# Kernel tuning notes

Measured on AMD Instinct MI355X. Metric: run time of the kernel, lower is better.

## Reference

```python
import jax, jax.numpy as jnp
import numpy as np

B, S, D = 2, 2048, 1024
H = 16
HD = D // H  # head_dim = 64


def setup_inputs() -> dict:
    key = jax.random.key(0)
    ks = jax.random.split(key, 9)
    sc_in = 1.0 / np.sqrt(D)
    return {
        "x": jax.random.normal(ks[0], (B, S, D), dtype=jnp.float32),
        "Wq": jax.random.normal(ks[1], (D, D), dtype=jnp.float32) * sc_in,
        "bq": jnp.zeros((D,), dtype=jnp.float32),
        "Wk": jax.random.normal(ks[2], (D, D), dtype=jnp.float32) * sc_in,
        "bk": jnp.zeros((D,), dtype=jnp.float32),
        "Wv": jax.random.normal(ks[3], (D, D), dtype=jnp.float32) * sc_in,
        "bv": jnp.zeros((D,), dtype=jnp.float32),
        "Wo": jax.random.normal(ks[4], (D, D), dtype=jnp.float32) * sc_in,
        "bo": jnp.zeros((D,), dtype=jnp.float32),
    }


def reference(x, Wq, bq, Wk, bk, Wv, bv, Wo, bo):
    # QKV projections: [B,S,D] -> [B,H,S,HD]
    def split_heads(t):
        return t.reshape(B, S, H, HD).transpose(0, 2, 1, 3)

    Q = split_heads(x @ Wq + bq)
    K = split_heads(x @ Wk + bk)
    V = split_heads(x @ Wv + bv)

    scale = 1.0 / np.sqrt(HD).astype(np.float32)
    scores = jnp.einsum("bhqd,bhkd->bhqk", Q, K) * scale  # [B,H,S,S]
    weights = jax.nn.softmax(scores, axis=-1)
    # dropout(p=0.1) is identity in eval mode
    attended = jnp.einsum("bhqk,bhkd->bhqd", weights, V)  # [B,H,S,HD]
    attended = attended.transpose(0, 2, 1, 3).reshape(B, S, D)
    return attended @ Wo + bo
```

## Files before the change

### kernel.cpp

```cpp
#include <hip/hip_runtime.h>
#include <hip/hip_bf16.h>


#define S_ 2048
#define D_ 1024
#define HD_ 64
#define LDSW 72
#define QSZ 4194304

typedef __attribute__((ext_vector_type(8))) short bf16x8;
typedef __attribute__((ext_vector_type(4))) float f32x4;

static __device__ __forceinline__ short f2bs(float f) {
    __hip_bfloat16 h = __float2bfloat16(f);
    return *reinterpret_cast<short*>(&h);
}
static __device__ __forceinline__ float bs2f(short s) {
    __hip_bfloat16 h = *reinterpret_cast<__hip_bfloat16*>(&s);
    return __bfloat162float(h);
}
static __device__ __forceinline__ bf16x8 cvt8(const float* p) {
    f32x4 u0 = *(const f32x4*)p;
    f32x4 u1 = *(const f32x4*)(p + 4);
    bf16x8 r;
    r[0] = f2bs(u0[0]); r[1] = f2bs(u0[1]); r[2] = f2bs(u0[2]); r[3] = f2bs(u0[3]);
    r[4] = f2bs(u1[0]); r[5] = f2bs(u1[1]); r[6] = f2bs(u1[2]); r[7] = f2bs(u1[3]);
    return r;
}
static __device__ __forceinline__ void gld16(const void* g, void* l) {
    __builtin_amdgcn_global_load_lds(
        (const __attribute__((address_space(1))) unsigned int*)g,
        (__attribute__((address_space(3))) unsigned int*)l, 16, 0, 0);
}
static __device__ __forceinline__ int detect_f32(const unsigned int* __restrict__ xw) {
    const unsigned int w = xw[threadIdx.x & 63];
    const int e = (int)((w >> 7) & 0xFFu);
    unsigned long long m = __ballot(e >= 117 && e <= 130);
    return (__popcll(m) >= 32) ? 0 : 1;
}

__global__ __launch_bounds__(256) void prep(
    const void* __restrict__ x,
    const void* __restrict__ w0, const void* __restrict__ w1,
    const void* __restrict__ w2, const void* __restrict__ w3,
    short* __restrict__ Wt, short* __restrict__ Xb)
{
    __shared__ __align__(16) short Ts[64 * LDSW];
    const int f32in = detect_f32((const unsigned int*)x);
    const int idx = blockIdx.x;

    if (idx >= 1024) {
        const int c = idx - 1024;
        const size_t base = (size_t)c * 8192 + (size_t)threadIdx.x * 8;
        if (f32in) {
            const float* xf = (const float*)x;
            #pragma unroll
            for (int i = 0; i < 4; ++i)
                *(bf16x8*)&Xb[base + (size_t)i * 2048] = cvt8(xf + base + (size_t)i * 2048);
        } else {
            const short* xs = (const short*)x;
            #pragma unroll
            for (int i = 0; i < 4; ++i)
                *(bf16x8*)&Xb[base + (size_t)i * 2048] = *(const bf16x8*)(xs + base + (size_t)i * 2048);
        }
        return;
    }

    const int z = idx >> 8, bb = idx & 255;
    const void* W = z == 0 ? w0 : z == 1 ? w1 : z == 2 ? w2 : w3;
    short* O = Wt + (size_t)z * D_ * D_;
    const int k0 = (bb & 15) * 64, n0 = (bb >> 4) * 64;
    const int t = threadIdx.x;
    const int row = t >> 2, seg = t & 3;

    if (f32in) {
        const float* wg = (const float*)W + (size_t)(k0 + row) * D_ + n0;
        *(bf16x8*)&Ts[row * LDSW + seg * 8]      = cvt8(wg + seg * 8);
        *(bf16x8*)&Ts[row * LDSW + seg * 8 + 32] = cvt8(wg + seg * 8 + 32);
    } else {
        const short* wg = (const short*)W + (size_t)(k0 + row) * D_ + n0;
        *(bf16x8*)&Ts[row * LDSW + seg * 8]      = *(const bf16x8*)(wg + seg * 8);
        *(bf16x8*)&Ts[row * LDSW + seg * 8 + 32] = *(const bf16x8*)(wg + seg * 8 + 32);
    }
    __syncthreads();

    short* og = O + (size_t)(n0 + row) * D_ + k0;
    #pragma unroll
    for (int g = 0; g < 2; ++g) {
        const int ks = seg * 8 + g * 32;
        alignas(16) short tmp[8];
        #pragma unroll
        for (int i = 0; i < 8; ++i) tmp[i] = Ts[(ks + i) * LDSW + row];
        *(bf16x8*)(og + ks) = *(const bf16x8*)tmp;
    }
}

__global__ __launch_bounds__(512) void gemm_qkv(
    const short* __restrict__ Xb, const short* __restrict__ Wt3,
    const void* __restrict__ bq, const void* __restrict__ bk,
    const void* __restrict__ bv, short* __restrict__ out,
    const unsigned int* __restrict__ xw)
{
    __shared__ __align__(16) short As[2][256 * 64];
    __shared__ __align__(16) short Bs[2][192 * 64];
    const int ext_f32 = detect_f32(xw);
    const int t = threadIdx.x;
    const int wave = t >> 6, lane = t & 63;
    const int quad = lane >> 4, l16 = lane & 15;
    const int wm = wave & 1, wn = wave >> 1;
    const int m0 = blockIdx.x * 256, n0 = blockIdx.y * 192;
    const int lr = lane >> 3;
    const int kx = ((lane & 7) ^ (lr & 7)) * 8;

    f32x4 acc[8][3];
    #pragma unroll
    for (int i = 0; i < 8; ++i)
        #pragma unroll
        for (int j = 0; j < 3; ++j) acc[i][j] = (f32x4){0.f, 0.f, 0.f, 0.f};

    const short* Ab = Xb  + (size_t)(m0 + wave * 32 + lr) * D_ + kx;
    const short* Bb = Wt3 + (size_t)(n0 + wave * 24 + lr) * D_ + kx;

    #pragma unroll
    for (int i = 0; i < 4; ++i)
        gld16(Ab + (size_t)i * 8 * D_, &As[0][(wave * 4 + i) * 512]);
    #pragma unroll
    for (int i = 0; i < 3; ++i)
        gld16(Bb + (size_t)i * 8 * D_, &Bs[0][(wave * 3 + i) * 512]);
    __syncthreads();

    for (int kb = 0; kb < 16; ++kb) {
        const int cur = kb & 1;
        if (kb < 15) {
            const int kn = (kb + 1) * 64;
            #pragma unroll
            for (int i = 0; i < 4; ++i)
                gld16(Ab + (size_t)i * 8 * D_ + kn, &As[cur ^ 1][(wave * 4 + i) * 512]);
            #pragma unroll
            for (int i = 0; i < 3; ++i)
                gld16(Bb + (size_t)i * 8 * D_ + kn, &Bs[cur ^ 1][(wave * 3 + i) * 512]);
        }

        #pragma unroll
        for (int ks = 0; ks < 2; ++ks) {
            const int sw = ((ks * 4 + quad) ^ (l16 & 7)) * 8;
            bf16x8 af[8], bfr[3];
            #pragma unroll
            for (int i = 0; i < 8; ++i)
                af[i]  = *(const bf16x8*)&As[cur][(wm * 128 + i * 16 + l16) * 64 + sw];
            #pragma unroll
            for (int i = 0; i < 3; ++i)
                bfr[i] = *(const bf16x8*)&Bs[cur][(wn * 48 + i * 16 + l16) * 64 + sw];
            #pragma unroll
            for (int mi = 0; mi < 8; ++mi)
                #pragma unroll
                for (int ni = 0; ni < 3; ++ni)
                    acc[mi][ni] = __builtin_amdgcn_mfma_f32_16x16x32_bf16(
                        af[mi], bfr[ni], acc[mi][ni], 0, 0, 0);
        }

        __syncthreads();
    }

    #pragma unroll
    for (int ni = 0; ni < 3; ++ni) {
        const int n = n0 + wn * 48 + ni * 16 + l16;
        const int id = n >> 10, nl = n & 1023, h = nl >> 6, d = nl & 63;
        const void* bias = id == 0 ? bq : id == 1 ? bk : bv;
        const float oscale = id == 0 ? 0.18033688011112042f : 1.0f;
        const float bvl = ext_f32 ? ((const float*)bias)[nl]
                                  : bs2f(((const short*)bias)[nl]);
        #pragma unroll
        for (int mi = 0; mi < 8; ++mi)
            #pragma unroll
            for (int r = 0; r < 4; ++r) {
                const int m = m0 + wm * 128 + mi * 16 + quad * 4 + r;
                const int b = m >> 11, s = m & 2047;
                const int bh = b * 16 + h;
                const float v = (acc[mi][ni][r] + bvl) * oscale;
                const size_t idx = (id < 2)
                    ? (size_t)id * QSZ + ((size_t)bh * S_ + s) * HD_ + d
                    : (size_t)2 * QSZ + ((size_t)bh * HD_ + d) * S_ + s;
                out[idx] = f2bs(v);
            }
    }
}

__global__ __launch_bounds__(256) void gemm_out(
    const short* __restrict__ A, const short* __restrict__ Bt,
    const void* __restrict__ bias, void* __restrict__ C,
    const unsigned int* __restrict__ xw)
{
    __shared__ __align__(16) short As[2][64 * 64];
    __shared__ __align__(16) short Bs[2][128 * 64];
    const int ext_f32 = detect_f32(xw);
    const int t = threadIdx.x;
    const int wave = t >> 6, lane = t & 63;
    const int quad = lane >> 4, l16 = lane & 15;
    const int wm = wave & 1, wn = wave >> 1;
    const int m0 = blockIdx.x * 64, n0 = blockIdx.y * 128;
    const int lr = lane >> 3;
    const int kx = ((lane & 7) ^ (lr & 7)) * 8;

    f32x4 acc[2][4];
    #pragma unroll
    for (int i = 0; i < 2; ++i)
        #pragma unroll
        for (int j = 0; j < 4; ++j) acc[i][j] = (f32x4){0.f, 0.f, 0.f, 0.f};

    const short* Ab = A  + (size_t)(m0 + wave * 16 + lr) * D_ + kx;
    const short* Bb = Bt + (size_t)(n0 + wave * 32 + lr) * D_ + kx;

    #pragma unroll
    for (int i = 0; i < 2; ++i)
        gld16(Ab + (size_t)i * 8 * D_, &As[0][(wave * 2 + i) * 512]);
    #pragma unroll
    for (int i = 0; i < 4; ++i)
        gld16(Bb + (size_t)i * 8 * D_, &Bs[0][(wave * 4 + i) * 512]);
    __syncthreads();

    for (int kb = 0; kb < 16; ++kb) {
        const int cur = kb & 1;
        if (kb < 15) {
            const int kn = (kb + 1) * 64;
            #pragma unroll
            for (int i = 0; i < 2; ++i)
                gld16(Ab + (size_t)i * 8 * D_ + kn, &As[cur ^ 1][(wave * 2 + i) * 512]);
            #pragma unroll
            for (int i = 0; i < 4; ++i)
                gld16(Bb + (size_t)i * 8 * D_ + kn, &Bs[cur ^ 1][(wave * 4 + i) * 512]);
        }

        #pragma unroll
        for (int ks = 0; ks < 2; ++ks) {
            const int sw = ((ks * 4 + quad) ^ (l16 & 7)) * 8;
            bf16x8 af[2], bfr[4];
            #pragma unroll
            for (int i = 0; i < 2; ++i)
                af[i] = *(const bf16x8*)&As[cur][(wm * 32 + i * 16 + l16) * 64 + sw];
            #pragma unroll
            for (int i = 0; i < 4; ++i)
                bfr[i] = *(const bf16x8*)&Bs[cur][(wn * 64 + i * 16 + l16) * 64 + sw];
            #pragma unroll
            for (int mi = 0; mi < 2; ++mi)
                #pragma unroll
                for (int ni = 0; ni < 4; ++ni)
                    acc[mi][ni] = __builtin_amdgcn_mfma_f32_16x16x32_bf16(
                        af[mi], bfr[ni], acc[mi][ni], 0, 0, 0);
        }

        __syncthreads();
    }

    #pragma unroll
    for (int ni = 0; ni < 4; ++ni) {
        const int n = n0 + wn * 64 + ni * 16 + l16;
        const float bvl = ext_f32 ? ((const float*)bias)[n]
                                  : bs2f(((const short*)bias)[n]);
        #pragma unroll
        for (int mi = 0; mi < 2; ++mi)
            #pragma unroll
            for (int r = 0; r < 4; ++r) {
                const int m = m0 + wm * 32 + mi * 16 + quad * 4 + r;
                const float v = acc[mi][ni][r] + bvl;
                const size_t idx = (size_t)m * D_ + n;
                if (ext_f32) ((float*)C)[idx] = v;
                else         ((short*)C)[idx] = f2bs(v);
            }
    }
}

__global__ __launch_bounds__(512) void attn(
    const short* __restrict__ Q, const short* __restrict__ K,
    const short* __restrict__ Vt, short* __restrict__ Aout)
{
    __shared__ __align__(16) short Ks[2][64 * 64];
    __shared__ __align__(16) short Vs[2][64 * 64];
    __shared__ __align__(16) short Ps[8][16 * LDSW];

    const int t = threadIdx.x;
    const int wave = t >> 6, lane = t & 63;
    const int quad = lane >> 4, l16 = lane & 15;
    const int bh = blockIdx.x;
    const int q0 = blockIdx.y * 128;
    const int lr = lane >> 3;
    const int kx = ((lane & 7) ^ (lr & 7)) * 8;
    short* pw = &Ps[wave][0];

    bf16x8 bq0, bq1;
    {
        const short* qr = Q + ((size_t)bh * S_ + q0 + wave * 16 + l16) * HD_ + quad * 8;
        bq0 = *(const bf16x8*)qr;
        bq1 = *(const bf16x8*)(qr + 32);
    }

    bf16x8 ones;
    #pragma unroll
    for (int i = 0; i < 8; ++i) ones[i] = (short)0x3F80;

    f32x4 o[4], lacc;
    lacc = (f32x4){0.f, 0.f, 0.f, 0.f};
    #pragma unroll
    for (int nt = 0; nt < 4; ++nt) o[nt] = (f32x4){0.f, 0.f, 0.f, 0.f};

    const short* Kb = K  + ((size_t)bh * S_  + wave * 8 + lr) * HD_ + kx;
    const short* Vb = Vt + ((size_t)bh * HD_ + wave * 8 + lr) * S_ + kx;

    gld16(Kb, &Ks[0][wave * 512]);
    gld16(Vb, &Vs[0][wave * 512]);
    __syncthreads();

    for (int j = 0; j < 32; ++j) {
        const int cur = j & 1;
        if (j < 31) {
            gld16(Kb + (size_t)((j + 1) * 64) * HD_, &Ks[cur ^ 1][wave * 512]);
            gld16(Vb + (j + 1) * 64,                 &Vs[cur ^ 1][wave * 512]);
        }

        f32x4 st[4];
        #pragma unroll
        for (int nt = 0; nt < 4; ++nt) {
            bf16x8 kf0 = *(const bf16x8*)&Ks[cur][(nt * 16 + l16) * 64 + ((quad ^ (l16 & 7)) * 8)];
            bf16x8 kf1 = *(const bf16x8*)&Ks[cur][(nt * 16 + l16) * 64 + (((4 + quad) ^ (l16 & 7)) * 8)];
            f32x4 z = (f32x4){0.f, 0.f, 0.f, 0.f};
            z = __builtin_amdgcn_mfma_f32_16x16x32_bf16(kf0, bq0, z, 0, 0, 0);
            z = __builtin_amdgcn_mfma_f32_16x16x32_bf16(kf1, bq1, z, 0, 0, 0);
            st[nt] = z;
        }

        #pragma unroll
        for (int nt = 0; nt < 4; ++nt) {
            unsigned u0 = __float_as_uint(__builtin_amdgcn_exp2f(st[nt][0]));
            unsigned u1 = __float_as_uint(__builtin_amdgcn_exp2f(st[nt][1]));
            unsigned u2 = __float_as_uint(__builtin_amdgcn_exp2f(st[nt][2]));
            unsigned u3 = __float_as_uint(__builtin_amdgcn_exp2f(st[nt][3]));
            uint2 pk;
            pk.x = __builtin_amdgcn_perm(u1, u0, 0x07060302);
            pk.y = __builtin_amdgcn_perm(u3, u2, 0x07060302);
            *(uint2*)&pw[l16 * LDSW + nt * 16 + quad * 4] = pk;
        }
        __builtin_amdgcn_s_waitcnt(0xc07f);

        #pragma unroll
        for (int ks = 0; ks < 2; ++ks) {
            bf16x8 vf[4];
            #pragma unroll
            for (int nt = 0; nt < 4; ++nt)
                vf[nt] = *(const bf16x8*)&Vs[cur][(nt * 16 + l16) * 64 + (((ks * 4 + quad) ^ (l16 & 7)) * 8)];
            bf16x8 ap = *(const bf16x8*)&pw[l16 * LDSW + ks * 32 + quad * 8];
            lacc = __builtin_amdgcn_mfma_f32_16x16x32_bf16(ap, ones, lacc, 0, 0, 0);
            #pragma unroll
            for (int nt = 0; nt < 4; ++nt)
                o[nt] = __builtin_amdgcn_mfma_f32_16x16x32_bf16(ap, vf[nt], o[nt], 0, 0, 0);
        }

        __syncthreads();
    }

    const int b = bh >> 4, h = bh & 15;
    #pragma unroll
    for (int r = 0; r < 4; ++r) {
        const float inv = 1.f / lacc[r];
        const int s = q0 + wave * 16 + quad * 4 + r;
        const size_t base = ((size_t)b * S_ + s) * D_ + h * HD_;
        #pragma unroll
        for (int nt = 0; nt < 4; ++nt)
            Aout[base + nt * 16 + l16] = f2bs(o[nt][r] * inv);
    }
}

extern "C" void kernel_launch(void* const* d_in, const int* in_sizes, int n_in,
                              void* d_out, int out_size, void* d_ws, size_t ws_size,
                              hipStream_t stream) {
    char* ws = (char*)d_ws;
    short* Wt  = (short*)(ws + ((size_t)1  << 20));
    short* Att = (short*)(ws + ((size_t)9  << 20));
    short* Xb  = Att;
    short* QKV = (short*)(ws + ((size_t)17 << 20));
    const unsigned int* xw = (const unsigned int*)d_in[0];

    prep<<<1536, 256, 0, stream>>>(d_in[0], d_in[1], d_in[3], d_in[5], d_in[7], Wt, Xb);
    gemm_qkv<<<dim3(16, 16), 512, 0, stream>>>(Xb, Wt, d_in[2], d_in[4], d_in[6], QKV, xw);
    attn<<<dim3(32, 16), 512, 0, stream>>>(QKV, QKV + QSZ, QKV + 2 * QSZ, Att);
    gemm_out<<<dim3(64, 8), 256, 0, stream>>>(Att, Wt + (3 << 20), d_in[8], d_out, xw);
}
```

Measured before the change: 203.8 us.

## Fuse all four stages into one persistent cooperative kernel with grid syncs

Replaces the four separate launches (weight/input prep, QKV GEMM, attention, output GEMM) with a single cooperative kernel of 256 blocks that runs each stage in turn, separated by grid-wide barriers. The aim is to remove per-launch overhead and inter-kernel gaps. In exchange, the grid is fixed at 256 blocks with one 512-thread block per CU and 112 KB of shared LDS. This lowers parallelism in stages that previously used more blocks (attention and the output GEMM each had 512), and the output GEMM now runs 512 threads on tiles sized for 256.

```diff
diff --git a/kernel.cpp b/kernel.cpp
--- a/kernel.cpp
+++ b/kernel.cpp
@@ -1,5 +1,8 @@
 #include <hip/hip_runtime.h>
+#include <hip/hip_cooperative_groups.h>
 #include <hip/hip_bf16.h>
+
+namespace cg = cooperative_groups;
 
 
 #define S_ 2048
@@ -39,333 +42,317 @@
     return (__popcll(m) >= 32) ? 0 : 1;
 }
 
-__global__ __launch_bounds__(256) void prep(
+__global__ __launch_bounds__(512, 1) void mha_fused(
     const void* __restrict__ x,
-    const void* __restrict__ w0, const void* __restrict__ w1,
-    const void* __restrict__ w2, const void* __restrict__ w3,
-    short* __restrict__ Wt, short* __restrict__ Xb)
+    const void* __restrict__ Wq, const void* __restrict__ Wk,
+    const void* __restrict__ Wv, const void* __restrict__ Wo,
+    const void* __restrict__ bq, const void* __restrict__ bk,
+    const void* __restrict__ bv, const void* __restrict__ bo,
+    void* __restrict__ Cout,
+    short* __restrict__ Wt, short* __restrict__ XbAtt, short* __restrict__ QKV)
 {
-    __shared__ __align__(16) short Ts[64 * LDSW];
+    __shared__ __align__(16) short SB[57344];
+    cg::grid_group grid = cg::this_grid();
+
+    const int t = threadIdx.x;
+    const int blk = blockIdx.x;
+    const int wave = t >> 6, lane = t & 63;
+    const int quad = lane >> 4, l16 = lane & 15;
+    const int lr = lane >> 3;
+    const int kx = ((lane & 7) ^ (lr & 7)) * 8;
     const int f32in = detect_f32((const unsigned int*)x);
-    const int idx = blockIdx.x;
-
-    if (idx >= 1024) {
-        const int c = idx - 1024;
-        const size_t base = (size_t)c * 8192 + (size_t)threadIdx.x * 8;
+
+    {
+        const int sub = t >> 8, tt = t & 255;
+        const int row = tt >> 2, seg = tt & 3;
+        short* Ts = &SB[sub * 4608];
+        #pragma unroll
+        for (int u = 0; u < 2; ++u) {
+            const int unit = blk * 4 + sub * 2 + u;
+            const int z = unit >> 8, bb = unit & 255;
+            const void* W = z == 0 ? Wq : z == 1 ? Wk : z == 2 ? Wv : Wo;
+            short* O = Wt + (size_t)z * D_ * D_;
+            const int k0 = (bb & 15) * 64, n0 = (bb >> 4) * 64;
+            if (u) __syncthreads();
+            if (f32in) {
+                const float* wg = (const float*)W + (size_t)(k0 + row) * D_ + n0;
+                *(bf16x8*)&Ts[row * LDSW + seg * 8]      = cvt8(wg + seg * 8);
+                *(bf16x8*)&Ts[row * LDSW + seg * 8 + 32] = cvt8(wg + seg * 8 + 32);
+            } else {
+                const short* wg = (const short*)W + (size_t)(k0 + row) * D_ + n0;
+                *(bf16x8*)&Ts[row * LDSW + seg * 8]      = *(const bf16x8*)(wg + seg * 8);
+                *(bf16x8*)&Ts[row * LDSW + seg * 8 + 32] = *(const bf16x8*)(wg + seg * 8 + 32);
+            }
+            __syncthreads();
+            short* og = O + (size_t)(n0 + row) * D_ + k0;
+            #pragma unroll
+            for (int g = 0; g < 2; ++g) {
+                const int ks = seg * 8 + g * 32;
+                alignas(16) short tmp[8];
+                #pragma unroll
+                for (int i = 0; i < 8; ++i) tmp[i] = Ts[(ks + i) * LDSW + row];
+                *(bf16x8*)(og + ks) = *(const bf16x8*)tmp;
+            }
+        }
+        const size_t base = (size_t)blk * 16384 + (size_t)t * 8;
         if (f32in) {
             const float* xf = (const float*)x;
             #pragma unroll
             for (int i = 0; i < 4; ++i)
-                *(bf16x8*)&Xb[base + (size_t)i * 2048] = cvt8(xf + base + (size_t)i * 2048);
+                *(bf16x8*)&XbAtt[base + (size_t)i * 4096] = cvt8(xf + base + (size_t)i * 4096);
         } else {
             const short* xs = (const short*)x;
             #pragma unroll
             for (int i = 0; i < 4; ++i)
-                *(bf16x8*)&Xb[base + (size_t)i * 2048] = *(const bf16x8*)(xs + base + (size_t)i * 2048);
-        }
-        return;
+                *(bf16x8*)&XbAtt[base + (size_t)i * 4096] = *(const bf16x8*)(xs + base + (size_t)i * 4096);
+        }
     }
-
-    const int z = idx >> 8, bb = idx & 255;
-    const void* W = z == 0 ? w0 : z == 1 ? w1 : z == 2 ? w2 : w3;
-    short* O = Wt + (size_t)z * D_ * D_;
-    const int k0 = (bb & 15) * 64, n0 = (bb >> 4) * 64;
-    const int t = threadIdx.x;
-    const int row = t >> 2, seg = t & 3;
-
-    if (f32in) {
-        const float* wg = (const float*)W + (size_t)(k0 + row) * D_ + n0;
-        *(bf16x8*)&Ts[row * LDSW + seg * 8]      = cvt8(wg + seg * 8);
-        *(bf16x8*)&Ts[row * LDSW + seg * 8 + 32] = cvt8(wg + seg * 8 + 32);
-    } else {
-        const short* wg = (const short*)W + (size_t)(k0 + row) * D_ + n0;
-        *(bf16x8*)&Ts[row * LDSW + seg * 8]      = *(const bf16x8*)(wg + seg * 8);
-        *(bf16x8*)&Ts[row * LDSW + seg * 8 + 32] = *(const bf16x8*)(wg + seg * 8 + 32);
+    grid.sync();
+
+    {
+        short* As = SB;
+        short* Bs = SB + 32768;
+        const int wm = wave & 1, wn = wave >> 1;
+        const int m0 = (blk & 15) * 256, n0 = (blk >> 4) * 192;
+
+        f32x4 acc[8][3];
+        #pragma unroll
+        for (int i = 0; i < 8; ++i)
+            #pragma unroll
+            for (int j = 0; j < 3; ++j) acc[i][j] = (f32x4){0.f, 0.f, 0.f, 0.f};
+
+        const short* Ab = XbAtt + (size_t)(m0 + wave * 32 + lr) * D_ + kx;
+        const short* Bb = Wt    + (size_t)(n0 + wave * 24 + lr) * D_ + kx;
+
+        #pragma unroll
+        for (int i = 0; i < 4; ++i)
+            gld16(Ab + (size_t)i * 8 * D_, &As[(wave * 4 + i) * 512]);
+        #pragma unroll
+        for (int i = 0; i < 3; ++i)
+            gld16(Bb + (size_t)i * 8 * D_, &Bs[(wave * 3 + i) * 512]);
+        __syncthreads();
+
+        for (int kb = 0; kb < 16; ++kb) {
+            const int cur = kb & 1;
+            if (kb < 15) {
+                const int kn = (kb + 1) * 64;
+                #pragma unroll
+                for (int i = 0; i < 4; ++i)
+                    gld16(Ab + (size_t)i * 8 * D_ + kn, &As[(cur ^ 1) * 16384 + (wave * 4 + i) * 512]);
+                #pragma unroll
+                for (int i = 0; i < 3; ++i)
+                    gld16(Bb + (size_t)i * 8 * D_ + kn, &Bs[(cur ^ 1) * 12288 + (wave * 3 + i) * 512]);
+            }
+            #pragma unroll
+            for (int ks = 0; ks < 2; ++ks) {
+                const int sw = ((ks * 4 + quad) ^ (l16 & 7)) * 8;
+                bf16x8 af[8], bfr[3];
+                #pragma unroll
+                for (int i = 0; i < 8; ++i)
+                    af[i]  = *(const bf16x8*)&As[cur * 16384 + (wm * 128 + i * 16 + l16) * 64 + sw];
+                #pragma unroll
+                for (int i = 0; i < 3; ++i)
+                    bfr[i] = *(const bf16x8*)&Bs[cur * 12288 + (wn * 48 + i * 16 + l16) * 64 + sw];
+                #pragma unroll
+                for (int mi = 0; mi < 8; ++mi)
+                    #pragma unroll
+                    for (int ni = 0; ni < 3; ++ni)
+                        acc[mi][ni] = __builtin_amdgcn_mfma_f32_16x16x32_bf16(
+                            af[mi], bfr[ni], acc[mi][ni], 0, 0, 0);
+            }
+            __syncthreads();
+        }
+
+        #pragma unroll
+        for (int ni = 0; ni < 3; ++ni) {
+            const int n = n0 + wn * 48 + ni * 16 + l16;
+            const int id = n >> 10, nl = n & 1023, h = nl >> 6, d = nl & 63;
+            const void* bias = id == 0 ? bq : id == 1 ? bk : bv;
+            const float oscale = id == 0 ? 0.18033688011112042f : 1.0f;
+            const float bvl = f32in ? ((const float*)bias)[nl]
+                                    : bs2f(((const short*)bias)[nl]);
+            #pragma unroll
+            for (int mi = 0; mi < 8; ++mi)
+                #pragma unroll
+                for (int r = 0; r < 4; ++r) {
+                    const int m = m0 + wm * 128 + mi * 16 + quad * 4 + r;
+                    const int b = m >> 11, s = m & 2047;
+                    const int bh = b * 16 + h;
+                    const float v = (acc[mi][ni][r] + bvl) * oscale;
+                    const size_t idx = (id < 2)
+                        ? (size_t)id * QSZ + ((size_t)bh * S_ + s) * HD_ + d
+                        : (size_t)2 * QSZ + ((size_t)bh * HD_ + d) * S_ + s;
+                    QKV[idx] = f2bs(v);
+                }
+        }
     }
-    __syncthreads();
-
-    short* og = O + (size_t)(n0 + row) * D_ + k0;
-    #pragma unroll
-    for (int g = 0; g < 2; ++g) {
-        const int ks = seg * 8 + g * 32;
-        alignas(16) short tmp[8];
-        #pragma unroll
-        for (int i = 0; i < 8; ++i) tmp[i] = Ts[(ks + i) * LDSW + row];
-        *(bf16x8*)(og + ks) = *(const bf16x8*)tmp;
+    grid.sync();
+
+    {
+        short* Ks = SB;
+        short* Vs = SB + 8192;
+        short* Ps = SB + 16384;
+        const short* Q  = QKV;
+        const short* K  = QKV + QSZ;
+        const short* Vt = QKV + 2 * QSZ;
+        short* pw = &Ps[wave * (16 * LDSW)];
+
+        #pragma unroll 1
+        for (int u = 0; u < 2; ++u) {
+            const int unit = blk * 2 + u;
+            const int bh = unit & 31, q0 = (unit >> 5) * 128;
+
+            bf16x8 bq0, bq1;
+            {
+                const short* qr = Q + ((size_t)bh * S_ + q0 + wave * 16 + l16) * HD_ + quad * 8;
+                bq0 = *(const bf16x8*)qr;
+                bq1 = *(const bf16x8*)(qr + 32);
+            }
+            bf16x8 ones;
+            #pragma unroll
+            for (int i = 0; i < 8; ++i) ones[i] = (short)0x3F80;
+
+            f32x4 o[4], lacc;
+            lacc = (f32x4){0.f, 0.f, 0.f, 0.f};
+            #pragma unroll
+            for (int nt = 0; nt < 4; ++nt) o[nt] = (f32x4){0.f, 0.f, 0.f, 0.f};
+
+            const short* Kb = K  + ((size_t)bh * S_  + wave * 8 + lr) * HD_ + kx;
+            const short* Vb = Vt + ((size_t)bh * HD_ + wave * 8 + lr) * S_ + kx;
+
+            gld16(Kb, &Ks[wave * 512]);
+            gld16(Vb, &Vs[wave * 512]);
+            __syncthreads();
+
+            for (int j = 0; j < 32; ++j) {
+                const int cur = j & 1;
+                if (j < 31) {
+                    gld16(Kb + (size_t)((j + 1) * 64) * HD_, &Ks[(cur ^ 1) * 4096 + wave * 512]);
+                    gld16(Vb + (j + 1) * 64,                 &Vs[(cur ^ 1) * 4096 + wave * 512]);
+                }
+
+                f32x4 st[4];
+                #pragma unroll
+                for (int nt = 0; nt < 4; ++nt) {
+                    bf16x8 kf0 = *(const bf16x8*)&Ks[cur * 4096 + (nt * 16 + l16) * 64 + ((quad ^ (l16 & 7)) * 8)];
+                    bf16x8 kf1 = *(const bf16x8*)&Ks[cur * 4096 + (nt * 16 + l16) * 64 + (((4 + quad) ^ (l16 & 7)) * 8)];
+                    f32x4 z = (f32x4){0.f, 0.f, 0.f, 0.f};
+                    z = __builtin_amdgcn_mfma_f32_16x16x32_bf16(kf0, bq0, z, 0, 0, 0);
+                    z = __builtin_amdgcn_mfma_f32_16x16x32_bf16(kf1, bq1, z, 0, 0, 0);
+                    st[nt] = z;
+                }
+
+                #pragma unroll
+                for (int nt = 0; nt < 4; ++nt) {
+                    unsigned u0 = __float_as_uint(__builtin_amdgcn_exp2f(st[nt][0]));
+                    unsigned u1 = __float_as_uint(__builtin_amdgcn_exp2f(st[nt][1]));
+                    unsigned u2 = __float_as_uint(__builtin_amdgcn_exp2f(st[nt][2]));
+                    unsigned u3 = __float_as_uint(__builtin_amdgcn_exp2f(st[nt][3]));
+                    uint2 pk;
+                    pk.x = __builtin_amdgcn_perm(u1, u0, 0x07060302);
+                    pk.y = __builtin_amdgcn_perm(u3, u2, 0x07060302);
+                    *(uint2*)&pw[l16 * LDSW + nt * 16 + quad * 4] = pk;
+                }
+                __builtin_amdgcn_s_waitcnt(0xc07f);
+
+                #pragma unroll
+                for (int ks = 0; ks < 2; ++ks) {
+                    bf16x8 vf[4];
+                    #pragma unroll
+                    for (int nt = 0; nt < 4; ++nt)
+                        vf[nt] = *(const bf16x8*)&Vs[cur * 4096 + (nt * 16 + l16) * 64 + (((ks * 4 + quad) ^ (l16 & 7)) * 8)];
+                    bf16x8 ap = *(const bf16x8*)&pw[l16 * LDSW + ks * 32 + quad * 8];
+                    lacc = __builtin_amdgcn_mfma_f32_16x16x32_bf16(ap, ones, lacc, 0, 0, 0);
+                    #pragma unroll
+                    for (int nt = 0; nt < 4; ++nt)
+                        o[nt] = __builtin_amdgcn_mfma_f32_16x16x32_bf16(ap, vf[nt], o[nt], 0, 0, 0);
+                }
+                __syncthreads();
+            }
+
+            const int b = bh >> 4, h = bh & 15;
+            #pragma unroll
+            for (int r = 0; r < 4; ++r) {
+                const float inv = 1.f / lacc[r];
+                const int s = q0 + wave * 16 + quad * 4 + r;
+                const size_t base = ((size_t)b * S_ + s) * D_ + h * HD_;
+                #pragma unroll
+                for (int nt = 0; nt < 4; ++nt)
+                    XbAtt[base + nt * 16 + l16] = f2bs(o[nt][r] * inv);
+            }
+        }
     }
-}
-
-__global__ __launch_bounds__(512) void gemm_qkv(
-    const short* __restrict__ Xb, const short* __restrict__ Wt3,
-    const void* __restrict__ bq, const void* __restrict__ bk,
-    const void* __restrict__ bv, short* __restrict__ out,
-    const unsigned int* __restrict__ xw)
-{
-    __shared__ __align__(16) short As[2][256 * 64];
-    __shared__ __align__(16) short Bs[2][192 * 64];
-    const int ext_f32 = detect_f32(xw);
-    const int t = threadIdx.x;
-    const int wave = t >> 6, lane = t & 63;
-    const int quad = lane >> 4, l16 = lane & 15;
-    const int wm = wave & 1, wn = wave >> 1;
-    const int m0 = blockIdx.x * 256, n0 = blockIdx.y * 192;
-    const int lr = lane >> 3;
-    const int kx = ((lane & 7) ^ (lr & 7)) * 8;
-
-    f32x4 acc[8][3];
-    #pragma unroll
-    for (int i = 0; i < 8; ++i)
-        #pragma unroll
-        for (int j = 0; j < 3; ++j) acc[i][j] = (f32x4){0.f, 0.f, 0.f, 0.f};
-
-    const short* Ab = Xb  + (size_t)(m0 + wave * 32 + lr) * D_ + kx;
-    const short* Bb = Wt3 + (size_t)(n0 + wave * 24 + lr) * D_ + kx;
-
-    #pragma unroll
-    for (int i = 0; i < 4; ++i)
-        gld16(Ab + (size_t)i * 8 * D_, &As[0][(wave * 4 + i) * 512]);
-    #pragma unroll
-    for (int i = 0; i < 3; ++i)
-        gld16(Bb + (size_t)i * 8 * D_, &Bs[0][(wave * 3 + i) * 512]);
-    __syncthreads();
-
-    for (int kb = 0; kb < 16; ++kb) {
-        const int cur = kb & 1;
-        if (kb < 15) {
-            const int kn = (kb + 1) * 64;
-            #pragma unroll
-            for (int i = 0; i < 4; ++i)
-                gld16(Ab + (size_t)i * 8 * D_ + kn, &As[cur ^ 1][(wave * 4 + i) * 512]);
-            #pragma unroll
-            for (int i = 0; i < 3; ++i)
-                gld16(Bb + (size_t)i * 8 * D_ + kn, &Bs[cur ^ 1][(wave * 3 + i) * 512]);
-        }
-
-        #pragma unroll
-        for (int ks = 0; ks < 2; ++ks) {
-            const int sw = ((ks * 4 + quad) ^ (l16 & 7)) * 8;
-            bf16x8 af[8], bfr[3];
-            #pragma unroll
-            for (int i = 0; i < 8; ++i)
-                af[i]  = *(const bf16x8*)&As[cur][(wm * 128 + i * 16 + l16) * 64 + sw];
-            #pragma unroll
-            for (int i = 0; i < 3; ++i)
-                bfr[i] = *(const bf16x8*)&Bs[cur][(wn * 48 + i * 16 + l16) * 64 + sw];
-            #pragma unroll
-            for (int mi = 0; mi < 8; ++mi)
-                #pragma unroll
-                for (int ni = 0; ni < 3; ++ni)
-                    acc[mi][ni] = __builtin_amdgcn_mfma_f32_16x16x32_bf16(
-                        af[mi], bfr[ni], acc[mi][ni], 0, 0, 0);
-        }
-
+    grid.sync();
+
+    {
+        short* As = SB;
+        short* Bs = SB + 16384;
+        const int wm = wave & 3, wn = wave >> 2;
+        const int m0 = (blk & 31) * 128, n0 = (blk >> 5) * 128;
+        const short* Bt = Wt + ((size_t)3 << 20);
+
+        f32x4 acc[2][4];
+        #pragma unroll
+        for (int i = 0; i < 2; ++i)
+            #pragma unroll
+            for (int j = 0; j < 4; ++j) acc[i][j] = (f32x4){0.f, 0.f, 0.f, 0.f};
+
+        const short* Ab = XbAtt + (size_t)(m0 + wave * 16 + lr) * D_ + kx;
+        const short* Bb = Bt    + (size_t)(n0 + wave * 16 + lr) * D_ + kx;
+
+        #pragma unroll
+        for (int i = 0; i < 2; ++i) {
+            gld16(Ab + (size_t)i * 8 * D_, &As[(wave * 2 + i) * 512]);
+            gld16(Bb + (size_t)i * 8 * D_, &Bs[(wave * 2 + i) * 512]);
+        }
         __syncthreads();
-    }
-
-    #pragma unroll
-    for (int ni = 0; ni < 3; ++ni) {
-        const int n = n0 + wn * 48 + ni * 16 + l16;
-        const int id = n >> 10, nl = n & 1023, h = nl >> 6, d = nl & 63;
-        const void* bias = id == 0 ? bq : id == 1 ? bk : bv;
-        const float oscale = id == 0 ? 0.18033688011112042f : 1.0f;
-        const float bvl = ext_f32 ? ((const float*)bias)[nl]
-                                  : bs2f(((const short*)bias)[nl]);
-        #pragma unroll
-        for (int mi = 0; mi < 8; ++mi)
-            #pragma unroll
-            for (int r = 0; r < 4; ++r) {
-                const int m = m0 + wm * 128 + mi * 16 + quad * 4 + r;
-                const int b = m >> 11, s = m & 2047;
-                const int bh = b * 16 + h;
-                const float v = (acc[mi][ni][r] + bvl) * oscale;
-                const size_t idx = (id < 2)
-                    ? (size_t)id * QSZ + ((size_t)bh * S_ + s) * HD_ + d
-                    : (size_t)2 * QSZ + ((size_t)bh * HD_ + d) * S_ + s;
-                out[idx] = f2bs(v);
-            }
-    }
-}
-
-__global__ __launch_bounds__(256) void gemm_out(
-    const short* __restrict__ A, const short* __restrict__ Bt,
-    const void* __restrict__ bias, void* __restrict__ C,
-    const unsigned int* __restrict__ xw)
-{
-    __shared__ __align__(16) short As[2][64 * 64];
-    __shared__ __align__(16) short Bs[2][128 * 64];
-    const int ext_f32 = detect_f32(xw);
-    const int t = threadIdx.x;
-    const int wave = t >> 6, lane = t & 63;
-    const int quad = lane >> 4, l16 = lane & 15;
-    const int wm = wave & 1, wn = wave >> 1;
-    const int m0 = blockIdx.x * 64, n0 = blockIdx.y * 128;
-    const int lr = lane >> 3;
-    const int kx = ((lane & 7) ^ (lr & 7)) * 8;
-
-    f32x4 acc[2][4];
-    #pragma unroll
-    for (int i = 0; i < 2; ++i)
-        #pragma unroll
-        for (int j = 0; j < 4; ++j) acc[i][j] = (f32x4){0.f, 0.f, 0.f, 0.f};
-
-    const short* Ab = A  + (size_t)(m0 + wave * 16 + lr) * D_ + kx;
-    const short* Bb = Bt + (size_t)(n0 + wave * 32 + lr) * D_ + kx;
-
-    #pragma unroll
-    for (int i = 0; i < 2; ++i)
-        gld16(Ab + (size_t)i * 8 * D_, &As[0][(wave * 2 + i) * 512]);
-    #pragma unroll
-    for (int i = 0; i < 4; ++i)
-        gld16(Bb + (size_t)i * 8 * D_, &Bs[0][(wave * 4 + i) * 512]);
-    __syncthreads();
-
-    for (int kb = 0; kb < 16; ++kb) {
-        const int cur = kb & 1;
-        if (kb < 15) {
-            const int kn = (kb + 1) * 64;
-            #pragma unroll
-            for (int i = 0; i < 2; ++i)
-                gld16(Ab + (size_t)i * 8 * D_ + kn, &As[cur ^ 1][(wave * 2 + i) * 512]);
-            #pragma unroll
-            for (int i = 0; i < 4; ++i)
-                gld16(Bb + (size_t)i * 8 * D_ + kn, &Bs[cur ^ 1][(wave * 4 + i) * 512]);
-        }
-
-        #pragma unroll
-        for (int ks = 0; ks < 2; ++ks) {
-            const int sw = ((ks * 4 + quad) ^ (l16 & 7)) * 8;
-            bf16x8 af[2], bfr[4];
-            #pragma unroll
-            for (int i = 0; i < 2; ++i)
-                af[i] = *(const bf16x8*)&As[cur][(wm * 32 + i * 16 + l16) * 64 + sw];
-            #pragma unroll
-            for (int i = 0; i < 4; ++i)
-                bfr[i] = *(const bf16x8*)&Bs[cur][(wn * 64 + i * 16 + l16) * 64 + sw];
+
+        for (int kb = 0; kb < 16; ++kb) {
+            const int cur = kb & 1;
+            if (kb < 15) {
+                const int kn = (kb + 1) * 64;
+                #pragma unroll
+                for (int i = 0; i < 2; ++i) {
+                    gld16(Ab + (size_t)i * 8 * D_ + kn, &As[(cur ^ 1) * 8192 + (wave * 2 + i) * 512]);
+                    gld16(Bb + (size_t)i * 8 * D_ + kn, &Bs[(cur ^ 1) * 8192 + (wave * 2 + i) * 512]);
+                }
+            }
+            #pragma unroll
+            for (int ks = 0; ks < 2; ++ks) {
+                const int sw = ((ks * 4 + quad) ^ (l16 & 7)) * 8;
+                bf16x8 af[2], bfr[4];
+                #pragma unroll
+                for (int i = 0; i < 2; ++i)
+                    af[i] = *(const bf16x8*)&As[cur * 8192 + (wm * 32 + i * 16 + l16) * 64 + sw];
+                #pragma unroll
+                for (int i = 0; i < 4; ++i)
+                    bfr[i] = *(const bf16x8*)&Bs[cur * 8192 + (wn * 64 + i * 16 + l16) * 64 + sw];
+                #pragma unroll
+                for (int mi = 0; mi < 2; ++mi)
+                    #pragma unroll
+                    for (int ni = 0; ni < 4; ++ni)
+                        acc[mi][ni] = __builtin_amdgcn_mfma_f32_16x16x32_bf16(
+                            af[mi], bfr[ni], acc[mi][ni], 0, 0, 0);
+            }
+            __syncthreads();
+        }
+
+        #pragma unroll
+        for (int ni = 0; ni < 4; ++ni) {
+            const int n = n0 + wn * 64 + ni * 16 + l16;
+            const float bvl = f32in ? ((const float*)bo)[n]
+                                    : bs2f(((const short*)bo)[n]);
             #pragma unroll
             for (int mi = 0; mi < 2; ++mi)
                 #pragma unroll
-                for (int ni = 0; ni < 4; ++ni)
-                    acc[mi][ni] = __builtin_amdgcn_mfma_f32_16x16x32_bf16(
-                        af[mi], bfr[ni], acc[mi][ni], 0, 0, 0);
-        }
-
-        __syncthreads();
-    }
-
-    #pragma unroll
-    for (int ni = 0; ni < 4; ++ni) {
-        const int n = n0 + wn * 64 + ni * 16 + l16;
-        const float bvl = ext_f32 ? ((const float*)bias)[n]
-                                  : bs2f(((const short*)bias)[n]);
-        #pragma unroll
-        for (int mi = 0; mi < 2; ++mi)
-            #pragma unroll
-            for (int r = 0; r < 4; ++r) {
-                const int m = m0 + wm * 32 + mi * 16 + quad * 4 + r;
-                const float v = acc[mi][ni][r] + bvl;
-                const size_t idx = (size_t)m * D_ + n;
-                if (ext_f32) ((float*)C)[idx] = v;
-                else         ((short*)C)[idx] = f2bs(v);
-            }
-    }
-}
-
-__global__ __launch_bounds__(512) void attn(
-    const short* __restrict__ Q, const short* __restrict__ K,
-    const short* __restrict__ Vt, short* __restrict__ Aout)
-{
-    __shared__ __align__(16) short Ks[2][64 * 64];
-    __shared__ __align__(16) short Vs[2][64 * 64];
-    __shared__ __align__(16) short Ps[8][16 * LDSW];
-
-    const int t = threadIdx.x;
-    const int wave = t >> 6, lane = t & 63;
-    const int quad = lane >> 4, l16 = lane & 15;
-    const int bh = blockIdx.x;
-    const int q0 = blockIdx.y * 128;
-    const int lr = lane >> 3;
-    const int kx = ((lane & 7) ^ (lr & 7)) * 8;
-    short* pw = &Ps[wave][0];
-
-    bf16x8 bq0, bq1;
-    {
-        const short* qr = Q + ((size_t)bh * S_ + q0 + wave * 16 + l16) * HD_ + quad * 8;
-        bq0 = *(const bf16x8*)qr;
-        bq1 = *(const bf16x8*)(qr + 32);
-    }
-
-    bf16x8 ones;
-    #pragma unroll
-    for (int i = 0; i < 8; ++i) ones[i] = (short)0x3F80;
-
-    f32x4 o[4], lacc;
-    lacc = (f32x4){0.f, 0.f, 0.f, 0.f};
-    #pragma unroll
-    for (int nt = 0; nt < 4; ++nt) o[nt] = (f32x4){0.f, 0.f, 0.f, 0.f};
-
-    const short* Kb = K  + ((size_t)bh * S_  + wave * 8 + lr) * HD_ + kx;
-    const short* Vb = Vt + ((size_t)bh * HD_ + wave * 8 + lr) * S_ + kx;
-
-    gld16(Kb, &Ks[0][wave * 512]);
-    gld16(Vb, &Vs[0][wave * 512]);
-    __syncthreads();
-
-    for (int j = 0; j < 32; ++j) {
-        const int cur = j & 1;
-        if (j < 31) {
-            gld16(Kb + (size_t)((j + 1) * 64) * HD_, &Ks[cur ^ 1][wave * 512]);
-            gld16(Vb + (j + 1) * 64,                 &Vs[cur ^ 1][wave * 512]);
-        }
-
-        f32x4 st[4];
-        #pragma unroll
-        for (int nt = 0; nt < 4; ++nt) {
-            bf16x8 kf0 = *(const bf16x8*)&Ks[cur][(nt * 16 + l16) * 64 + ((quad ^ (l16 & 7)) * 8)];
-            bf16x8 kf1 = *(const bf16x8*)&Ks[cur][(nt * 16 + l16) * 64 + (((4 + quad) ^ (l16 & 7)) * 8)];
-            f32x4 z = (f32x4){0.f, 0.f, 0.f, 0.f};
-            z = __builtin_amdgcn_mfma_f32_16x16x32_bf16(kf0, bq0, z, 0, 0, 0);
-            z = __builtin_amdgcn_mfma_f32_16x16x32_bf16(kf1, bq1, z, 0, 0, 0);
-            st[nt] = z;
-        }
-
-        #pragma unroll
-        for (int nt = 0; nt < 4; ++nt) {
-            unsigned u0 = __float_as_uint(__builtin_amdgcn_exp2f(st[nt][0]));
-            unsigned u1 = __float_as_uint(__builtin_amdgcn_exp2f(st[nt][1]));
-            unsigned u2 = __float_as_uint(__builtin_amdgcn_exp2f(st[nt][2]));
-            unsigned u3 = __float_as_uint(__builtin_amdgcn_exp2f(st[nt][3]));
-            uint2 pk;
-            pk.x = __builtin_amdgcn_perm(u1, u0, 0x07060302);
-            pk.y = __builtin_amdgcn_perm(u3, u2, 0x07060302);
-            *(uint2*)&pw[l16 * LDSW + nt * 16 + quad * 4] = pk;
-        }
-        __builtin_amdgcn_s_waitcnt(0xc07f);
-
-        #pragma unroll
-        for (int ks = 0; ks < 2; ++ks) {
-            bf16x8 vf[4];
-            #pragma unroll
-            for (int nt = 0; nt < 4; ++nt)
-                vf[nt] = *(const bf16x8*)&Vs[cur][(nt * 16 + l16) * 64 + (((ks * 4 + quad) ^ (l16 & 7)) * 8)];
-            bf16x8 ap = *(const bf16x8*)&pw[l16 * LDSW + ks * 32 + quad * 8];
-            lacc = __builtin_amdgcn_mfma_f32_16x16x32_bf16(ap, ones, lacc, 0, 0, 0);
-            #pragma unroll
-            for (int nt = 0; nt < 4; ++nt)
-                o[nt] = __builtin_amdgcn_mfma_f32_16x16x32_bf16(ap, vf[nt], o[nt], 0, 0, 0);
-        }
-
-        __syncthreads();
-    }
-
-    const int b = bh >> 4, h = bh & 15;
-    #pragma unroll
-    for (int r = 0; r < 4; ++r) {
-        const float inv = 1.f / lacc[r];
-        const int s = q0 + wave * 16 + quad * 4 + r;
-        const size_t base = ((size_t)b * S_ + s) * D_ + h * HD_;
-        #pragma unroll
-        for (int nt = 0; nt < 4; ++nt)
-            Aout[base + nt * 16 + l16] = f2bs(o[nt][r] * inv);
+                for (int r = 0; r < 4; ++r) {
+                    const int m = m0 + wm * 32 + mi * 16 + quad * 4 + r;
+                    const float v = acc[mi][ni][r] + bvl;
+                    const size_t idx = (size_t)m * D_ + n;
+                    if (f32in) ((float*)Cout)[idx] = v;
+                    else       ((short*)Cout)[idx] = f2bs(v);
+                }
+        }
     }
 }
 
@@ -373,14 +360,19 @@
                               void* d_out, int out_size, void* d_ws, size_t ws_size,
                               hipStream_t stream) {
     char* ws = (char*)d_ws;
-    short* Wt  = (short*)(ws + ((size_t)1  << 20));
-    short* Att = (short*)(ws + ((size_t)9  << 20));
-    short* Xb  = Att;
-    short* QKV = (short*)(ws + ((size_t)17 << 20));
-    const unsigned int* xw = (const unsigned int*)d_in[0];
-
-    prep<<<1536, 256, 0, stream>>>(d_in[0], d_in[1], d_in[3], d_in[5], d_in[7], Wt, Xb);
-    gemm_qkv<<<dim3(16, 16), 512, 0, stream>>>(Xb, Wt, d_in[2], d_in[4], d_in[6], QKV, xw);
-    attn<<<dim3(32, 16), 512, 0, stream>>>(QKV, QKV + QSZ, QKV + 2 * QSZ, Att);
-    gemm_out<<<dim3(64, 8), 256, 0, stream>>>(Att, Wt + (3 << 20), d_in[8], d_out, xw);
-}
+    short* Wt    = (short*)(ws + ((size_t)1  << 20));
+    short* XbAtt = (short*)(ws + ((size_t)9  << 20));
+    short* QKV   = (short*)(ws + ((size_t)17 << 20));
+
+    void* x  = d_in[0];
+    void* Wq = d_in[1]; void* bq = d_in[2];
+    void* Wk = d_in[3]; void* bk = d_in[4];
+    void* Wv = d_in[5]; void* bv = d_in[6];
+    void* Wo = d_in[7]; void* bo = d_in[8];
+    void* Co = d_out;
+
+    void* args[] = { &x, &Wq, &Wk, &Wv, &Wo, &bq, &bk, &bv, &bo, &Co,
+                     &Wt, &XbAtt, &QKV };
+    hipLaunchCooperativeKernel((void*)mha_fused, dim3(256), dim3(512),
+                               args, 0, stream);
+}
```

Result: slower. 329.7 us (+61.8%).
